# Performance work log

Measured on AMD Instinct MI355X. Metric: run time of the kernel, lower is better.

## Reference

```python
import jax, jax.numpy as jnp
import numpy as np

B, N, M = 8, 2048, 32768          # batch, queries, buffer size
QD = 512                          # query_dim / context dim
DR, DL = 256, 256                 # buffer_dims (reps, labels)
D = DR + DL
H, DH = 8, 64                     # heads, dim_head
INNER = H * DH
SCALE = DH ** -0.5


def setup_inputs() -> dict:
    key = jax.random.key(0)
    ks = jax.random.split(key, 8)
    return {
        "x": jax.random.normal(ks[0], (B, N, QD), jnp.float32),
        "context": jax.random.normal(ks[1], (B, M, D), jnp.float32),
        "Wq": jax.random.normal(ks[2], (QD, INNER), jnp.float32) * 0.02,
        "Wk": jax.random.normal(ks[3], (DL, INNER), jnp.float32) * 0.02,
        "Wv": jax.random.normal(ks[4], (DR, INNER), jnp.float32) * 0.02,
        "We": jax.random.normal(ks[5], (INNER, DR), jnp.float32) * 0.02,
        "Wout": jax.random.normal(ks[6], (INNER, QD), jnp.float32) * 0.02,
        "bout": jnp.zeros((QD,), jnp.float32),
        "topk": 8,
    }


def reference(x, context, Wq, Wk, Wv, We, Wout, bout, topk):
    b, n, _ = x.shape
    q = x @ Wq                                   # [b, n, INNER]
    emb = q @ We                                 # [b, n, DR]
    # Original loop always uses embedding[:, 0, :] for every position i,
    # so retrieval is identical across the sequence; compute once, broadcast.
    e0 = emb[:, 0, :]                            # [b, DR]
    buf_reps = context[..., :DR]                 # [b, m, DR]
    dist = jnp.linalg.norm(buf_reps - e0[:, None, :], axis=-1)  # [b, m]
    _, idx = jax.lax.top_k(-dist, topk)          # smallest-distance indices [b, topk]
    ctx = jnp.take_along_axis(context, idx[:, :, None], axis=1)  # [b, topk, D]
    ctx = jnp.broadcast_to(ctx[:, None], (b, n, topk, D))        # [b, n, topk, D]
    # attn_retrieval == 'reps_for_v': k from labels, v from reps
    reps, labels = ctx[..., :DR], ctx[..., DR:]
    k = labels @ Wk                              # [b, n, topk, INNER]
    v = reps @ Wv                                # [b, n, topk, INNER]
    qh = q.reshape(b, n, H, DH)
    kh = k.reshape(b, n, topk, H, DH)
    vh = v.reshape(b, n, topk, H, DH)
    sim = jnp.einsum('bnhd,bnjhd->bhnj', qh, kh) * SCALE
    attn = jax.nn.softmax(sim, axis=-1)
    out = jnp.einsum('bhnj,bnjhd->bnhd', attn, vh).reshape(b, n, INNER)
    return out @ Wout + bout
```

## Files before the change

kernel.cpp:

```cpp
#include <hip/hip_runtime.h>
#include <hip/hip_bf16.h>

#define BB 8
#define NN 2048
#define MM 32768
#define QD 512
#define DRR 256
#define DDL 256
#define DD 512
#define HH 8
#define DHH 64
#define INNERD 512
#define TOPK 8
#define SCALE 0.125f

typedef float f32x4 __attribute__((ext_vector_type(4)));
typedef __bf16 bf16x8 __attribute__((ext_vector_type(8)));

#define OFF_Q0P  0
#define OFF_E0P  32768
#define OFF_KS   49152
#define OFF_VS   81920
#define OFF_DIST 114688
#define OFF_IDX  376832
#define OFF_WQP_BYTES 1507584
#define OFF_WOP_BYTES 2031872

__device__ __forceinline__ unsigned short f2bf(float f) {
  unsigned int u = __float_as_uint(f);
  unsigned int r = (u + 0x7FFFu + ((u >> 16) & 1u)) >> 16;
  return (unsigned short)r;
}
__device__ __forceinline__ float bf2f(unsigned int us) {
  return __uint_as_float(us << 16);
}
__device__ __forceinline__ unsigned int pk2(float a, float b) {
  return (unsigned int)f2bf(a) | ((unsigned int)f2bf(b) << 16);
}
__device__ __forceinline__ void unpk8(uint4 v, float* o) {
  o[0] = bf2f(v.x & 0xffffu); o[1] = bf2f(v.x >> 16);
  o[2] = bf2f(v.y & 0xffffu); o[3] = bf2f(v.y >> 16);
  o[4] = bf2f(v.z & 0xffffu); o[5] = bf2f(v.z >> 16);
  o[6] = bf2f(v.w & 0xffffu); o[7] = bf2f(v.w >> 16);
}

__global__ void k_wprep(const float* __restrict__ W, unsigned short* __restrict__ dst) {
  int f = blockIdx.x * 256 + threadIdx.x;
  int lane = f & 63, nt = (f >> 6) & 31, kb = f >> 11;
  int kbase = kb * 32 + (lane >> 4) * 8;
  int n = nt * 16 + (lane & 15);
  unsigned short o8[8];
#pragma unroll
  for (int j = 0; j < 8; ++j) o8[j] = f2bf(W[(size_t)(kbase + j) * 512 + n]);
  uint4 v = make_uint4((unsigned)o8[0] | ((unsigned)o8[1] << 16),
                       (unsigned)o8[2] | ((unsigned)o8[3] << 16),
                       (unsigned)o8[4] | ((unsigned)o8[5] << 16),
                       (unsigned)o8[6] | ((unsigned)o8[7] << 16));
  *(uint4*)(dst + (size_t)f * 8) = v;
}

__global__ void k_q0(const float* __restrict__ x, const float* __restrict__ Wq,
                     float* __restrict__ q0p) {
  int b = blockIdx.x, g = blockIdx.y;
  __shared__ float xs[64];
  int tid = threadIdx.x;
  if (tid < 64) xs[tid] = x[(size_t)b * NN * QD + g * 64 + tid];
  __syncthreads();
  float acc = 0.f;
  const float* wp = Wq + (size_t)(g * 64) * 512 + tid;
#pragma unroll 8
  for (int c = 0; c < 64; ++c) acc += xs[c] * wp[(size_t)c * 512];
  q0p[g * 4096 + b * 512 + tid] = acc;
}

__global__ void k_e0(const float* __restrict__ q0p, const float* __restrict__ We,
                     float* __restrict__ e0p) {
  int b = blockIdx.x, gi = blockIdx.y;
  __shared__ float qs[64];
  int tid = threadIdx.x;
  if (tid < 64) {
    float s = 0.f;
#pragma unroll
    for (int g = 0; g < 8; ++g) s += q0p[g * 4096 + b * 512 + gi * 64 + tid];
    qs[tid] = s;
  }
  __syncthreads();
  float acc = 0.f;
  const float* wp = We + (size_t)(gi * 64) * 256 + tid;
#pragma unroll 8
  for (int c = 0; c < 64; ++c) acc += qs[c] * wp[(size_t)c * 256];
  e0p[gi * 2048 + b * 256 + tid] = acc;
}

__global__ void k_dist(const float* __restrict__ ctx, const float* __restrict__ e0p,
                       float* __restrict__ dist) {
  __shared__ float es[256];
  int tid = threadIdx.x;
  int row0 = blockIdx.x * 4;
  int b = row0 >> 15;
  {
    float s = 0.f;
#pragma unroll
    for (int g = 0; g < 8; ++g) s += e0p[g * 2048 + b * 256 + tid];
    es[tid] = s;
  }
  __syncthreads();
  int w = tid >> 6, l = tid & 63;
  int row = row0 + w;
  float4 c = ((const float4*)(ctx + (size_t)row * DD))[l];
  float4 e = ((const float4*)es)[l];
  float dx = c.x - e.x, dy = c.y - e.y, dz = c.z - e.z, dw = c.w - e.w;
  float s = dx * dx + dy * dy + dz * dz + dw * dw;
#pragma unroll
  for (int m = 1; m < 64; m <<= 1) s += __shfl_xor(s, m, 64);
  if (l == 0) dist[row] = s;
}

__global__ void k_topk(const float* __restrict__ dist, int* __restrict__ idxo) {
  int b = blockIdx.x, tid = threadIdx.x;
  const float* dp = dist + (size_t)b * MM;
  float lv[8]; int li[8];
#pragma unroll
  for (int i = 0; i < 8; ++i) { lv[i] = INFINITY; li[i] = 1 << 30; }
  for (int t = 0; t < MM / 256; ++t) {
    int m = t * 256 + tid;
    float v = dp[m];
    if (v < lv[7]) {
      int p = 7;
      while (p > 0 && lv[p - 1] > v) { lv[p] = lv[p - 1]; li[p] = li[p - 1]; --p; }
      lv[p] = v; li[p] = m;
    }
  }
  __shared__ float wvs[4];
  __shared__ int wis[4];
  __shared__ int winS;
  int head = 0;
  for (int r = 0; r < 8; ++r) {
    float cv = (head < 8) ? lv[head] : INFINITY;
    int ci = (head < 8) ? li[head] : (1 << 30);
#pragma unroll
    for (int m = 1; m < 64; m <<= 1) {
      float ov = __shfl_xor(cv, m, 64);
      int oi = __shfl_xor(ci, m, 64);
      if (ov < cv || (ov == cv && oi < ci)) { cv = ov; ci = oi; }
    }
    int w = tid >> 6;
    if ((tid & 63) == 0) { wvs[w] = cv; wis[w] = ci; }
    __syncthreads();
    if (tid == 0) {
      float bv = wvs[0]; int bi = wis[0];
#pragma unroll
      for (int k = 1; k < 4; ++k)
        if (wvs[k] < bv || (wvs[k] == bv && wis[k] < bi)) { bv = wvs[k]; bi = wis[k]; }
      winS = bi;
      idxo[b * 8 + r] = bi;
    }
    __syncthreads();
    if (head < 8 && li[head] == winS) ++head;
    __syncthreads();
  }
}

__global__ void k_kv(const float* __restrict__ ctx, const int* __restrict__ idx,
                     const float* __restrict__ Wk, const float* __restrict__ Wv,
                     float* __restrict__ ks, float* __restrict__ vs) {
  int b = blockIdx.x, ic = blockIdx.y, cc = blockIdx.z;
  int tid = threadIdx.x;
  __shared__ float rep[8][64], lab[8][64];
  __shared__ int ids[8];
  if (tid < 8) ids[tid] = idx[b * 8 + tid];
  __syncthreads();
  for (int e = tid; e < 512; e += 128) {
    int j = e >> 6, c = e & 63;
    const float* rowp = ctx + ((size_t)b * MM + ids[j]) * DD + cc * 64;
    rep[j][c] = rowp[c];
    lab[j][c] = rowp[256 + c];
  }
  __syncthreads();
  int i = ic * 128 + tid;
  float ka[8] = {0, 0, 0, 0, 0, 0, 0, 0}, va[8] = {0, 0, 0, 0, 0, 0, 0, 0};
  for (int c = 0; c < 64; ++c) {
    float wk = Wk[(size_t)(cc * 64 + c) * 512 + i];
    float wv = Wv[(size_t)(cc * 64 + c) * 512 + i];
#pragma unroll
    for (int j = 0; j < 8; ++j) { ka[j] += lab[j][c] * wk; va[j] += rep[j][c] * wv; }
  }
#pragma unroll
  for (int j = 0; j < 8; ++j) {
    atomicAdd(&ks[((size_t)b * 8 + j) * 512 + i], ka[j]);
    atomicAdd(&vs[((size_t)b * 8 + j) * 512 + i], va[j]);
  }
}

__device__ __forceinline__ void gemm512(const unsigned short* aT, const unsigned short* wP,
                                        int w, int l, f32x4 (&acc)[2][8]) {
  int quad = l >> 4, lcol = l & 15;
#pragma unroll 4
  for (int kb = 0; kb < 16; ++kb) {
    uint4 a0 = *(const uint4*)(aT + (size_t)lcol * 520 + kb * 32 + quad * 8);
    uint4 a1 = *(const uint4*)(aT + (size_t)(16 + lcol) * 520 + kb * 32 + quad * 8);
    bf16x8 af0 = __builtin_bit_cast(bf16x8, a0);
    bf16x8 af1 = __builtin_bit_cast(bf16x8, a1);
    const uint4* bp = (const uint4*)(wP + ((size_t)(kb * 32 + w * 8) * 64 + l) * 8);
#pragma unroll
    for (int t = 0; t < 8; ++t) {
      bf16x8 bf = __builtin_bit_cast(bf16x8, bp[(size_t)t * 64]);
      acc[0][t] = __builtin_amdgcn_mfma_f32_16x16x32_bf16(af0, bf, acc[0][t], 0, 0, 0);
      acc[1][t] = __builtin_amdgcn_mfma_f32_16x16x32_bf16(af1, bf, acc[1][t], 0, 0, 0);
    }
  }
}

__global__ __launch_bounds__(256, 2) void k_fused(
    const float* __restrict__ x, const unsigned short* __restrict__ wqP,
    const unsigned short* __restrict__ woP, const float* __restrict__ ks,
    const float* __restrict__ vs, const float* __restrict__ bout,
    float* __restrict__ out) {
  __shared__ unsigned short aT[32 * 520];
  __shared__ unsigned short ksl[8 * 520];
  __shared__ unsigned short vsl[8 * 520];
  int tid = threadIdx.x;
  int tok0 = blockIdx.x * 32;
  int b = tok0 >> 11;

  for (int e = tid; e < 4096; e += 256) {
    int j = e >> 9, i = e & 511;
    int h = i >> 6, d = i & 63;
    ksl[h * 520 + j * 64 + d] = f2bf(ks[((size_t)b * 8 + j) * 512 + i]);
    vsl[h * 520 + j * 64 + d] = f2bf(vs[((size_t)b * 8 + j) * 512 + i]);
  }
#pragma unroll
  for (int it = 0; it < 8; ++it) {
    int g = it * 256 + tid;
    int k8 = g & 63, m = g >> 6;
    const float* xp = x + ((size_t)(tok0 + m)) * 512 + k8 * 8;
    float4 a = ((const float4*)xp)[0];
    float4 c = ((const float4*)xp)[1];
    uint4 pk = make_uint4(pk2(a.x, a.y), pk2(a.z, a.w), pk2(c.x, c.y), pk2(c.z, c.w));
    *(uint4*)(aT + (size_t)m * 520 + k8 * 8) = pk;
  }
  __syncthreads();

  int w = tid >> 6, l = tid & 63;
  int quad = l >> 4, lcol = l & 15;
  f32x4 acc[2][8];
#pragma unroll
  for (int mt = 0; mt < 2; ++mt)
#pragma unroll
    for (int t = 0; t < 8; ++t) acc[mt][t] = (f32x4){0.f, 0.f, 0.f, 0.f};

  gemm512(aT, wqP, w, l, acc);
  __syncthreads();

#pragma unroll
  for (int mt = 0; mt < 2; ++mt)
#pragma unroll
    for (int t = 0; t < 8; ++t)
#pragma unroll
      for (int r = 0; r < 4; ++r) {
        int mrow = mt * 16 + quad * 4 + r;
        int col = w * 128 + t * 16 + lcol;
        aT[(size_t)mrow * 520 + col] = f2bf(acc[mt][t][r]);
      }
  __syncthreads();

  {
    int m = tid >> 3, h = tid & 7;
    float sim[8] = {0, 0, 0, 0, 0, 0, 0, 0};
#pragma unroll
    for (int dc0 = 0; dc0 < 4; ++dc0) {
      int dc = (dc0 + h) & 3;
      float qf[16];
      const uint4* qp = (const uint4*)(aT + (size_t)m * 520 + h * 64 + dc * 16);
      unpk8(qp[0], qf); unpk8(qp[1], qf + 8);
#pragma unroll
      for (int j = 0; j < 8; ++j) {
        const uint4* kp = (const uint4*)(ksl + (size_t)h * 520 + j * 64 + dc * 16);
        float kf[16];
        unpk8(kp[0], kf); unpk8(kp[1], kf + 8);
        float s = 0.f;
#pragma unroll
        for (int i = 0; i < 16; ++i) s += qf[i] * kf[i];
        sim[j] += s;
      }
    }
    float z[8], mx = -INFINITY;
#pragma unroll
    for (int j = 0; j < 8; ++j) { z[j] = sim[j] * SCALE; mx = fmaxf(mx, z[j]); }
    float p[8], psum = 0.f;
#pragma unroll
    for (int j = 0; j < 8; ++j) { p[j] = __expf(z[j] - mx); psum += p[j]; }
    float inv = 1.f / psum;
#pragma unroll
    for (int j = 0; j < 8; ++j) p[j] *= inv;
#pragma unroll
    for (int dc0 = 0; dc0 < 4; ++dc0) {
      int dc = (dc0 + h) & 3;
      float o16[16];
#pragma unroll
      for (int i = 0; i < 16; ++i) o16[i] = 0.f;
#pragma unroll
      for (int j = 0; j < 8; ++j) {
        const uint4* vp = (const uint4*)(vsl + (size_t)h * 520 + j * 64 + dc * 16);
        float vf[16];
        unpk8(vp[0], vf); unpk8(vp[1], vf + 8);
#pragma unroll
        for (int i = 0; i < 16; ++i) o16[i] += p[j] * vf[i];
      }
      uint4 o0 = make_uint4(pk2(o16[0], o16[1]), pk2(o16[2], o16[3]),
                            pk2(o16[4], o16[5]), pk2(o16[6], o16[7]));
      uint4 o1 = make_uint4(pk2(o16[8], o16[9]), pk2(o16[10], o16[11]),
                            pk2(o16[12], o16[13]), pk2(o16[14], o16[15]));
      uint4* op = (uint4*)(aT + (size_t)m * 520 + h * 64 + dc * 16);
      op[0] = o0; op[1] = o1;
    }
  }
  __syncthreads();

#pragma unroll
  for (int mt = 0; mt < 2; ++mt)
#pragma unroll
    for (int t = 0; t < 8; ++t) acc[mt][t] = (f32x4){0.f, 0.f, 0.f, 0.f};
  gemm512(aT, woP, w, l, acc);

#pragma unroll
  for (int t = 0; t < 8; ++t) {
    int col = w * 128 + t * 16 + lcol;
    float bb = bout[col];
#pragma unroll
    for (int mt = 0; mt < 2; ++mt)
#pragma unroll
      for (int r = 0; r < 4; ++r) {
        int mrow = mt * 16 + quad * 4 + r;
        out[((size_t)(tok0 + mrow)) * 512 + col] = acc[mt][t][r] + bb;
      }
  }
}

extern "C" void kernel_launch(void* const* d_in, const int* in_sizes, int n_in,
                              void* d_out, int out_size, void* d_ws, size_t ws_size,
                              hipStream_t stream) {
  const float* x    = (const float*)d_in[0];
  const float* ctx  = (const float*)d_in[1];
  const float* Wq   = (const float*)d_in[2];
  const float* Wk   = (const float*)d_in[3];
  const float* Wv   = (const float*)d_in[4];
  const float* We   = (const float*)d_in[5];
  const float* Wout = (const float*)d_in[6];
  const float* bout = (const float*)d_in[7];
  float* out = (float*)d_out;
  float* ws = (float*)d_ws;

  float* q0p  = ws + OFF_Q0P;
  float* e0p  = ws + OFF_E0P;
  float* ks   = ws + OFF_KS;
  float* vs   = ws + OFF_VS;
  float* dist = ws + OFF_DIST;
  int*   idx  = (int*)(ws + OFF_IDX);
  unsigned short* wqP = (unsigned short*)((char*)d_ws + OFF_WQP_BYTES);
  unsigned short* woP = (unsigned short*)((char*)d_ws + OFF_WOP_BYTES);

  hipMemsetAsync((char*)d_ws + (size_t)OFF_KS * 4, 0, (size_t)65536 * 4, stream);

  k_wprep<<<128, 256, 0, stream>>>(Wq, wqP);
  k_wprep<<<128, 256, 0, stream>>>(Wout, woP);
  k_q0<<<dim3(8, 8), 512, 0, stream>>>(x, Wq, q0p);
  k_e0<<<dim3(8, 8), 256, 0, stream>>>(q0p, We, e0p);
  k_dist<<<65536, 256, 0, stream>>>(ctx, e0p, dist);
  k_topk<<<8, 256, 0, stream>>>(dist, idx);
  k_kv<<<dim3(8, 4, 4), 128, 0, stream>>>(ctx, idx, Wk, Wv, ks, vs);
  k_fused<<<512, 256, 0, stream>>>(x, wqP, woP, ks, vs, bout, out);
}
```

Baseline: 854.0 us.

## Fuse prep kernels, merge top-k with K/V projection, drop atomics and memset

Merges the two weight-prep launches into one and reduces the e0 partials once in a dedicated kernel, so the distance kernel just loads e0. The distance kernel now processes 16 rows per block instead of 4. Top-k selection and the K/V projection run in one 512-thread kernel per batch that writes K/V directly, which removes the memset, the atomics and two launches. The fused top-k/KV kernel runs on only 8 blocks, so its serial per-block work may grow.

New measurement: 907.3 us. 1.06x slower.

```diff
diff --git a/kernel.cpp b/kernel.cpp
--- a/kernel.cpp
+++ b/kernel.cpp
@@ -18,11 +18,10 @@
 typedef __bf16 bf16x8 __attribute__((ext_vector_type(8)));
 
 #define OFF_Q0P  0
-#define OFF_E0P  32768
-#define OFF_KS   49152
-#define OFF_VS   81920
+#define OFF_E0   32768
+#define OFF_KS   40960
+#define OFF_VS   73728
 #define OFF_DIST 114688
-#define OFF_IDX  376832
 #define OFF_WQP_BYTES 1507584
 #define OFF_WOP_BYTES 2031872
 
@@ -44,8 +43,12 @@
   o[6] = bf2f(v.w & 0xffffu); o[7] = bf2f(v.w >> 16);
 }
 
-__global__ void k_wprep(const float* __restrict__ W, unsigned short* __restrict__ dst) {
-  int f = blockIdx.x * 256 + threadIdx.x;
+__global__ void k_wprep2(const float* __restrict__ Wq, const float* __restrict__ Wo,
+                         unsigned short* __restrict__ dq, unsigned short* __restrict__ dof) {
+  int bid = blockIdx.x;
+  const float* W = (bid < 128) ? Wq : Wo;
+  unsigned short* dst = (bid < 128) ? dq : dof;
+  int f = (bid & 127) * 256 + threadIdx.x;
   int lane = f & 63, nt = (f >> 6) & 31, kb = f >> 11;
   int kbase = kb * 32 + (lane >> 4) * 8;
   int n = nt * 16 + (lane & 15);
@@ -73,57 +76,64 @@
   q0p[g * 4096 + b * 512 + tid] = acc;
 }
 
-__global__ void k_e0(const float* __restrict__ q0p, const float* __restrict__ We,
-                     float* __restrict__ e0p) {
-  int b = blockIdx.x, gi = blockIdx.y;
-  __shared__ float qs[64];
+__global__ void k_e0f(const float* __restrict__ q0p, const float* __restrict__ We,
+                      float* __restrict__ e0) {
+  int b = blockIdx.x, rc = blockIdx.y;
+  __shared__ float q0s[512];
+  __shared__ float red[4][64];
   int tid = threadIdx.x;
+  for (int i = tid; i < 512; i += 256) {
+    float s = 0.f;
+#pragma unroll
+    for (int g = 0; g < 8; ++g) s += q0p[g * 4096 + b * 512 + i];
+    q0s[i] = s;
+  }
+  __syncthreads();
+  int ic = tid >> 6, rl = tid & 63;
+  float acc = 0.f;
+  const float* wp = We + (size_t)(ic * 128) * 256 + rc * 64 + rl;
+#pragma unroll 8
+  for (int c = 0; c < 128; ++c) acc += q0s[ic * 128 + c] * wp[(size_t)c * 256];
+  red[ic][rl] = acc;
+  __syncthreads();
   if (tid < 64) {
-    float s = 0.f;
-#pragma unroll
-    for (int g = 0; g < 8; ++g) s += q0p[g * 4096 + b * 512 + gi * 64 + tid];
-    qs[tid] = s;
-  }
-  __syncthreads();
-  float acc = 0.f;
-  const float* wp = We + (size_t)(gi * 64) * 256 + tid;
-#pragma unroll 8
-  for (int c = 0; c < 64; ++c) acc += qs[c] * wp[(size_t)c * 256];
-  e0p[gi * 2048 + b * 256 + tid] = acc;
-}
-
-__global__ void k_dist(const float* __restrict__ ctx, const float* __restrict__ e0p,
+    float s = red[0][tid] + red[1][tid] + red[2][tid] + red[3][tid];
+    e0[b * 256 + rc * 64 + tid] = s;
+  }
+}
+
+__global__ void k_dist(const float* __restrict__ ctx, const float* __restrict__ e0,
                        float* __restrict__ dist) {
   __shared__ float es[256];
   int tid = threadIdx.x;
-  int row0 = blockIdx.x * 4;
-  int b = row0 >> 15;
-  {
-    float s = 0.f;
-#pragma unroll
-    for (int g = 0; g < 8; ++g) s += e0p[g * 2048 + b * 256 + tid];
-    es[tid] = s;
-  }
+  int row0 = blockIdx.x * 16;
+  int b = blockIdx.x >> 11;
+  es[tid] = e0[b * 256 + tid];
   __syncthreads();
   int w = tid >> 6, l = tid & 63;
-  int row = row0 + w;
-  float4 c = ((const float4*)(ctx + (size_t)row * DD))[l];
   float4 e = ((const float4*)es)[l];
-  float dx = c.x - e.x, dy = c.y - e.y, dz = c.z - e.z, dw = c.w - e.w;
-  float s = dx * dx + dy * dy + dz * dz + dw * dw;
-#pragma unroll
-  for (int m = 1; m < 64; m <<= 1) s += __shfl_xor(s, m, 64);
-  if (l == 0) dist[row] = s;
-}
-
-__global__ void k_topk(const float* __restrict__ dist, int* __restrict__ idxo) {
+#pragma unroll
+  for (int rr = 0; rr < 4; ++rr) {
+    int row = row0 + rr * 4 + w;
+    float4 c = ((const float4*)(ctx + (size_t)row * DD))[l];
+    float dx = c.x - e.x, dy = c.y - e.y, dz = c.z - e.z, dw = c.w - e.w;
+    float s = dx * dx + dy * dy + dz * dz + dw * dw;
+#pragma unroll
+    for (int m = 1; m < 64; m <<= 1) s += __shfl_xor(s, m, 64);
+    if (l == 0) dist[row] = s;
+  }
+}
+
+__global__ void k_topkkv(const float* __restrict__ dist, const float* __restrict__ ctx,
+                         const float* __restrict__ Wk, const float* __restrict__ Wv,
+                         float* __restrict__ ks, float* __restrict__ vs) {
   int b = blockIdx.x, tid = threadIdx.x;
   const float* dp = dist + (size_t)b * MM;
   float lv[8]; int li[8];
 #pragma unroll
   for (int i = 0; i < 8; ++i) { lv[i] = INFINITY; li[i] = 1 << 30; }
-  for (int t = 0; t < MM / 256; ++t) {
-    int m = t * 256 + tid;
+  for (int t = 0; t < MM / 512; ++t) {
+    int m = t * 512 + tid;
     float v = dp[m];
     if (v < lv[7]) {
       int p = 7;
@@ -131,8 +141,9 @@
       lv[p] = v; li[p] = m;
     }
   }
-  __shared__ float wvs[4];
-  __shared__ int wis[4];
+  __shared__ float wvs[8];
+  __shared__ int wis[8];
+  __shared__ int ids[8];
   __shared__ int winS;
   int head = 0;
   for (int r = 0; r < 8; ++r) {
@@ -150,45 +161,39 @@
     if (tid == 0) {
       float bv = wvs[0]; int bi = wis[0];
 #pragma unroll
-      for (int k = 1; k < 4; ++k)
+      for (int k = 1; k < 8; ++k)
         if (wvs[k] < bv || (wvs[k] == bv && wis[k] < bi)) { bv = wvs[k]; bi = wis[k]; }
       winS = bi;
-      idxo[b * 8 + r] = bi;
+      ids[r] = bi;
     }
     __syncthreads();
     if (head < 8 && li[head] == winS) ++head;
     __syncthreads();
   }
-}
-
-__global__ void k_kv(const float* __restrict__ ctx, const int* __restrict__ idx,
-                     const float* __restrict__ Wk, const float* __restrict__ Wv,
-                     float* __restrict__ ks, float* __restrict__ vs) {
-  int b = blockIdx.x, ic = blockIdx.y, cc = blockIdx.z;
-  int tid = threadIdx.x;
-  __shared__ float rep[8][64], lab[8][64];
-  __shared__ int ids[8];
-  if (tid < 8) ids[tid] = idx[b * 8 + tid];
-  __syncthreads();
-  for (int e = tid; e < 512; e += 128) {
-    int j = e >> 6, c = e & 63;
-    const float* rowp = ctx + ((size_t)b * MM + ids[j]) * DD + cc * 64;
-    rep[j][c] = rowp[c];
-    lab[j][c] = rowp[256 + c];
-  }
-  __syncthreads();
-  int i = ic * 128 + tid;
+
+  __shared__ float labrep[8][512];
+#pragma unroll
+  for (int e = tid, it = 0; it < 8; ++it, e += 512) {
+    int j = e >> 9, c = e & 511;
+    labrep[j][c] = ctx[((size_t)b * MM + ids[j]) * DD + c];
+  }
+  __syncthreads();
+  int i = tid;
   float ka[8] = {0, 0, 0, 0, 0, 0, 0, 0}, va[8] = {0, 0, 0, 0, 0, 0, 0, 0};
-  for (int c = 0; c < 64; ++c) {
-    float wk = Wk[(size_t)(cc * 64 + c) * 512 + i];
-    float wv = Wv[(size_t)(cc * 64 + c) * 512 + i];
-#pragma unroll
-    for (int j = 0; j < 8; ++j) { ka[j] += lab[j][c] * wk; va[j] += rep[j][c] * wv; }
+#pragma unroll 4
+  for (int c = 0; c < 256; ++c) {
+    float wk = Wk[(size_t)c * 512 + i];
+    float wv = Wv[(size_t)c * 512 + i];
+#pragma unroll
+    for (int j = 0; j < 8; ++j) {
+      ka[j] += labrep[j][256 + c] * wk;
+      va[j] += labrep[j][c] * wv;
+    }
   }
 #pragma unroll
   for (int j = 0; j < 8; ++j) {
-    atomicAdd(&ks[((size_t)b * 8 + j) * 512 + i], ka[j]);
-    atomicAdd(&vs[((size_t)b * 8 + j) * 512 + i], va[j]);
+    ks[((size_t)b * 8 + j) * 512 + i] = ka[j];
+    vs[((size_t)b * 8 + j) * 512 + i] = va[j];
   }
 }
 
@@ -352,22 +357,17 @@
   float* ws = (float*)d_ws;
 
   float* q0p  = ws + OFF_Q0P;
-  float* e0p  = ws + OFF_E0P;
+  float* e0   = ws + OFF_E0;
   float* ks   = ws + OFF_KS;
   float* vs   = ws + OFF_VS;
   float* dist = ws + OFF_DIST;
-  int*   idx  = (int*)(ws + OFF_IDX);
   unsigned short* wqP = (unsigned short*)((char*)d_ws + OFF_WQP_BYTES);
   unsigned short* woP = (unsigned short*)((char*)d_ws + OFF_WOP_BYTES);
 
-  hipMemsetAsync((char*)d_ws + (size_t)OFF_KS * 4, 0, (size_t)65536 * 4, stream);
-
-  k_wprep<<<128, 256, 0, stream>>>(Wq, wqP);
-  k_wprep<<<128, 256, 0, stream>>>(Wout, woP);
+  k_wprep2<<<256, 256, 0, stream>>>(Wq, Wout, wqP, woP);
   k_q0<<<dim3(8, 8), 512, 0, stream>>>(x, Wq, q0p);
-  k_e0<<<dim3(8, 8), 256, 0, stream>>>(q0p, We, e0p);
-  k_dist<<<65536, 256, 0, stream>>>(ctx, e0p, dist);
-  k_topk<<<8, 256, 0, stream>>>(dist, idx);
-  k_kv<<<dim3(8, 4, 4), 128, 0, stream>>>(ctx, idx, Wk, Wv, ks, vs);
+  k_e0f<<<dim3(8, 4), 256, 0, stream>>>(q0p, We, e0);
+  k_dist<<<16384, 256, 0, stream>>>(ctx, e0, dist);
+  k_topkkv<<<8, 512, 0, stream>>>(dist, ctx, Wk, Wv, ks, vs);
   k_fused<<<512, 256, 0, stream>>>(x, wqP, woP, ks, vs, bout, out);
 }
```
